# Kernel tuning notes

Hardware: AMD Instinct MI355X
Metric: run time of the kernel (lower is better)

The kernel has to match this reference:

```python
import jax, jax.numpy as jnp
import numpy as np
from jax import lax

K = 3          # kernel_size
OUT = 256      # out_channels
IN_CPG = 256   # in_channels // groups
GROUPS = 1
STRIDE = 1
PAD = 1
DN = ('NCHW', 'OIHW', 'NCHW')


def _bounds(i, n, o):
    return int(np.floor(i * n / o)), int(np.ceil((i + 1) * n / o))


def adaptive_pool2d(x, o, reduce_fn):
    # Faithful torch AdaptiveAvg/MaxPool2d: static bin boundaries.
    H, W = x.shape[2], x.shape[3]
    rows = []
    for i in range(o):
        r0, r1 = _bounds(i, H, o)
        cells = []
        for j in range(o):
            c0, c1 = _bounds(j, W, o)
            cells.append(reduce_fn(x[:, :, r0:r1, c0:c1], axis=(2, 3)))
        rows.append(jnp.stack(cells, axis=-1))
    return jnp.stack(rows, axis=-2)  # (B, C, o, o)


def _gconv(x, w, fg, pad='VALID'):
    return lax.conv_general_dilated(x, w, (1, 1), pad,
                                    dimension_numbers=DN,
                                    feature_group_count=fg)


def setup_inputs() -> dict:
    key = jax.random.key(0)
    ks = jax.random.split(key, 7)
    s = 0.05
    return {
        'x':     jax.random.normal(ks[0], (32, 256, 56, 56), jnp.float32),
        'w1':    jax.random.normal(ks[1], (IN_CPG, GROUPS, 3, 3), jnp.float32) * s,
        'b1':    jax.random.normal(ks[2], (IN_CPG,), jnp.float32) * s,
        'w2':    jax.random.normal(ks[3], (OUT * IN_CPG, 1, 1, 1), jnp.float32) * s,
        'b2':    jax.random.normal(ks[4], (OUT * IN_CPG,), jnp.float32) * s,
        'w_att': jax.random.normal(ks[5], (OUT * IN_CPG, GROUPS, 3, 3), jnp.float32) * s,
        'b_att': jax.random.normal(ks[6], (OUT * IN_CPG,), jnp.float32) * s,
    }


def reference(x, w1, b1, w2, b2, w_att, b_att):
    B, C, H, W = x.shape
    # attention branch: maxpool -> grouped 3x3 conv -> sigmoid
    maxi = adaptive_pool2d(x, K + 2, jnp.max)                    # (B, C, K+2, K+2)
    att = _gconv(maxi, w_att, IN_CPG) + b_att[None, :, None, None]  # (B, OUT*IN_CPG, K, K)
    att = jax.nn.sigmoid(att).reshape(B * OUT, IN_CPG, K, K)
    # weight branch: avgpool -> depthwise 3x3 -> relu -> grouped 1x1
    avg = adaptive_pool2d(x, K + 2, jnp.mean)                    # (B, C, K+2, K+2)
    wgt = jax.nn.relu(_gconv(avg, w1, IN_CPG) + b1[None, :, None, None])  # (B, IN_CPG, K, K)
    wgt = _gconv(wgt, w2, IN_CPG) + b2[None, :, None, None]      # (B, OUT*IN_CPG, K, K)
    wgt = wgt.reshape(B * OUT, IN_CPG, K, K)
    # per-sample dynamic conv as grouped conv with batch-as-groups
    xg = x.reshape(1, B * C, H, W)
    out = lax.conv_general_dilated(xg, wgt * att, (STRIDE, STRIDE),
                                   [(PAD, PAD), (PAD, PAD)],
                                   dimension_numbers=DN,
                                   feature_group_count=GROUPS * B)
    return out.reshape(B, OUT, out.shape[-2], out.shape[-1])
```

## Files before the change

kernel.cpp:

```cpp
#include <hip/hip_runtime.h>
#include <hip/hip_bf16.h>

#define BATCH 32
#define CIN   256
#define OCH   256
#define HW    56
#define PW    58
#define PAREA (PW*PW)
#define PLANE (HW*HW)

typedef float float4v __attribute__((ext_vector_type(4)));
typedef short short8  __attribute__((ext_vector_type(8)));
typedef short short4v __attribute__((ext_vector_type(4)));

__device__ __forceinline__ unsigned short f2bf(float f) {
  union { float f; unsigned u; } v; v.f = f;
  unsigned r = v.u + 0x7fffu + ((v.u >> 16) & 1u);
  return (unsigned short)(r >> 16);
}

__device__ __forceinline__ void gll16(const unsigned short* g, unsigned short* l) {
  __builtin_amdgcn_global_load_lds(
      (const __attribute__((address_space(1))) void*)g,
      (__attribute__((address_space(3))) void*)l,
      16, 0, 0);
}

__global__ __launch_bounds__(512) void poolprep_kernel(
    const float* __restrict__ x, float* __restrict__ avgp,
    float* __restrict__ maxp, unsigned short* __restrict__ xp) {
  __shared__ float pl[4][3140];
  int p = blockIdx.x;
  int L = (p & 7) * 256 + (p >> 3);
  int cg = L & 63, b = L >> 6;
  int tid = threadIdx.x;
  const float* src = x + ((size_t)(b * 256 + cg * 4)) * PLANE;

  float4v v[7];
#pragma unroll
  for (int k = 0; k < 7; ++k) {
    int e = tid + k * 512;
    if (e < 3136) v[k] = *(const float4v*)&src[(size_t)(e / 784) * PLANE + (e % 784) * 4];
  }
#pragma unroll
  for (int k = 0; k < 7; ++k) {
    int e = tid + k * 512;
    if (e < 3136) *(float4v*)&pl[e / 784][(e % 784) * 4] = v[k];
  }
  __syncthreads();

  if (tid < 100) {
    int c = tid / 25, bin = tid % 25;
    int i = bin / 5, j = bin % 5;
    int r0 = (i * HW) / 5, r1 = ((i + 1) * HW + 4) / 5;
    int c0 = (j * HW) / 5, c1 = ((j + 1) * HW + 4) / 5;
    float s = 0.f, m = -1e30f;
    for (int r = r0; r < r1; ++r)
      for (int c2 = c0; c2 < c1; ++c2) {
        float vv = pl[c][r * HW + c2];
        s += vv; m = fmaxf(m, vv);
      }
    size_t o = ((size_t)(b * 256 + cg * 4 + c)) * 25 + bin;
    avgp[o] = s / (float)((r1 - r0) * (c1 - c0));
    maxp[o] = m;
  }

  int ch0 = cg * 4;
  int g32 = ch0 >> 5;
  int cc = (ch0 >> 3) & 3;
  int half = (ch0 >> 2) & 1;
  for (int pi = tid; pi < PLANE; pi += 512) {
    int y = pi / 56, col = pi % 56;
    int pos = (y + 1) * PW + (col + 1);
    short4v w4;
#pragma unroll
    for (int k = 0; k < 4; ++k) w4[k] = (short)f2bf(pl[k][pi]);
    int cph = cc ^ ((pos >> 1) & 3);
    *(short4v*)&xp[((size_t)b * PAREA + pos) * 256 + g32 * 32 + cph * 8 + half * 4] = w4;
  }
}

__global__ __launch_bounds__(256) void wcalc_kernel(
    const float* __restrict__ avgp, const float* __restrict__ maxp,
    const float* __restrict__ w1, const float* __restrict__ b1,
    const float* __restrict__ w2, const float* __restrict__ b2,
    const float* __restrict__ watt, const float* __restrict__ batt,
    unsigned short* __restrict__ Wbf) {
  int blk = blockIdx.x;
  int oc = blk & 255, b = blk >> 8;
  __shared__ float s_avg[25], s_max[25], s_w1[9], s_wgt1[9];
  int tid = threadIdx.x;
  size_t base = ((size_t)b * 256 + oc) * 25;
  if (tid < 25) { s_avg[tid] = avgp[base + tid]; s_max[tid] = maxp[base + tid]; }
  if (tid >= 32 && tid < 41) s_w1[tid - 32] = w1[oc * 9 + (tid - 32)];
  __syncthreads();
  if (tid < 9) {
    int ky = tid / 3, kx = tid % 3;
    float acc = b1[oc];
    for (int u = 0; u < 3; ++u)
      for (int v = 0; v < 3; ++v)
        acc += s_avg[(ky + u) * 5 + kx + v] * s_w1[u * 3 + v];
    s_wgt1[tid] = fmaxf(acc, 0.f);
  }
  __syncthreads();
  int ic = tid;
  size_t g = (size_t)oc * 256 + ic;
  float wa[9];
#pragma unroll
  for (int r = 0; r < 9; ++r) wa[r] = watt[g * 9 + r];
  float ba = batt[g], w2v = w2[g], b2v = b2[g];

  int ocb = oc >> 7, ocl = oc & 127;
  int icb = ic >> 5;
  size_t tilebase = ((size_t)((b * 2 + ocb) * 8 + icb)) * 9;
  size_t elem = (size_t)ocl * 32 + (ic & 31);

#pragma unroll
  for (int r = 0; r < 9; ++r) {
    int ky = r / 3, kx = r % 3;
    float s = ba;
#pragma unroll
    for (int u = 0; u < 3; ++u)
#pragma unroll
      for (int v = 0; v < 3; ++v)
        s += s_max[(ky + u) * 5 + kx + v] * wa[u * 3 + v];
    float att = 1.f / (1.f + __expf(-s));
    float wv = (s_wgt1[r] * w2v + b2v) * att;
    Wbf[(tilebase + r) * 4096 + elem] = f2bf(wv);
  }
}

__global__ __launch_bounds__(256) void border_kernel(unsigned short* __restrict__ xp) {
  int bid = blockIdx.x;
  int b = bid / 228, bi = bid % 228;
  int pos;
  if (bi < 58)       pos = bi;
  else if (bi < 116) pos = 57 * PW + (bi - 58);
  else if (bi < 172) pos = (bi - 116 + 1) * PW;
  else               pos = (bi - 172 + 1) * PW + 57;
  xp[((size_t)b * PAREA + pos) * 256 + threadIdx.x] = 0;
}

__global__ __launch_bounds__(256, 2) void conv_kernel(
    const unsigned short* __restrict__ xp,
    const unsigned short* __restrict__ Wbf,
    float* __restrict__ out) {
  __shared__ unsigned short bpl[2][348 * 32];

  int p = blockIdx.x;
  int L = (p & 7) * 112 + (p >> 3);
  int rt = L % 14; int t2 = L / 14; int ocb = t2 & 1; int b = t2 >> 1;
  int y0 = rt * 4;
  int tid = threadIdx.x;
  int lane = tid & 63, w = tid >> 6;
  int mw = w & 1, nw = w >> 1;
  int quad = lane >> 4, l16 = lane & 15;

  int basepos[7];
#pragma unroll
  for (int nt = 0; nt < 7; ++nt) {
    int n = nw * 112 + nt * 16 + l16;
    basepos[nt] = (n / 56) * PW + (n % 56);
  }

  float4v acc[4][7];
#pragma unroll
  for (int mt = 0; mt < 4; ++mt)
#pragma unroll
    for (int nt = 0; nt < 7; ++nt)
      acc[mt][nt] = (float4v){0.f, 0.f, 0.f, 0.f};

  const size_t xbase = ((size_t)b * PAREA + (size_t)y0 * PW) * 256;
  const unsigned short* wb = Wbf + (size_t)((b * 2 + ocb) * 72) * 4096;
  const int aoff = (mw * 64 + l16) * 32 + quad * 8;

  for (int e = tid; e < 1392; e += 256)
    gll16(&xp[xbase + (size_t)(e >> 2) * 256 + (e & 3) * 8], &bpl[0][e * 8]);
  short8 af0, af1, af2, af3, an0, an1, an2, an3;
  {
    const unsigned short* w0p = wb + aoff;
    af0 = *(const short8*)&w0p[0];    af1 = *(const short8*)&w0p[512];
    af2 = *(const short8*)&w0p[1024]; af3 = *(const short8*)&w0p[1536];
    const unsigned short* w1p = wb + 4096 + aoff;
    an0 = *(const short8*)&w1p[0];    an1 = *(const short8*)&w1p[512];
    an2 = *(const short8*)&w1p[1024]; an3 = *(const short8*)&w1p[1536];
  }
  __syncthreads();

#define RSTEP(R, ICB, CUR, DO2) do {                                            \
    const int _po = ((R) / 3) * PW + ((R) % 3);                                 \
    _Pragma("unroll")                                                           \
    for (int nt = 0; nt < 7; ++nt) {                                            \
      int pr = basepos[nt] + _po;                                               \
      short8 _bf = *(const short8*)&bpl[CUR][pr * 32 + ((quad ^ ((pr >> 1) & 3)) << 3)]; \
      acc[0][nt] = __builtin_amdgcn_mfma_f32_16x16x32_bf16(af0, _bf, acc[0][nt], 0, 0, 0); \
      acc[1][nt] = __builtin_amdgcn_mfma_f32_16x16x32_bf16(af1, _bf, acc[1][nt], 0, 0, 0); \
      acc[2][nt] = __builtin_amdgcn_mfma_f32_16x16x32_bf16(af2, _bf, acc[2][nt], 0, 0, 0); \
      acc[3][nt] = __builtin_amdgcn_mfma_f32_16x16x32_bf16(af3, _bf, acc[3][nt], 0, 0, 0); \
    }                                                                           \
    af0 = an0; af1 = an1; af2 = an2; af3 = an3;                                 \
    if (DO2) {                                                                  \
      const unsigned short* _w = wb + (size_t)((ICB) * 9 + (R) + 2) * 4096 + aoff; \
      an0 = *(const short8*)&_w[0];    an1 = *(const short8*)&_w[512];          \
      an2 = *(const short8*)&_w[1024]; an3 = *(const short8*)&_w[1536];         \
    }                                                                           \
  } while (0)

#pragma unroll 1
  for (int icb = 0; icb < 7; ++icb) {
    int cur = icb & 1;
    for (int e = tid; e < 1392; e += 256)
      gll16(&xp[xbase + (size_t)(e >> 2) * 256 + (icb + 1) * 32 + (e & 3) * 8],
            &bpl[cur ^ 1][e * 8]);
    RSTEP(0, icb, cur, 1); RSTEP(1, icb, cur, 1); RSTEP(2, icb, cur, 1);
    RSTEP(3, icb, cur, 1); RSTEP(4, icb, cur, 1); RSTEP(5, icb, cur, 1);
    RSTEP(6, icb, cur, 1); RSTEP(7, icb, cur, 1); RSTEP(8, icb, cur, 1);
    __syncthreads();
  }
  RSTEP(0, 7, 1, 1); RSTEP(1, 7, 1, 1); RSTEP(2, 7, 1, 1);
  RSTEP(3, 7, 1, 1); RSTEP(4, 7, 1, 1); RSTEP(5, 7, 1, 1);
  RSTEP(6, 7, 1, 1); RSTEP(7, 7, 1, 0); RSTEP(8, 7, 1, 0);
#undef RSTEP

#pragma unroll
  for (int mt = 0; mt < 4; ++mt) {
    int m = ocb * 128 + mw * 64 + mt * 16 + quad * 4;
#pragma unroll
    for (int nt = 0; nt < 7; ++nt) {
      int n = nw * 112 + nt * 16 + l16;
      int yy = y0 + n / 56, xx = n % 56;
      size_t o = (((size_t)b * 256 + m) * 56 + yy) * 56 + xx;
#pragma unroll
      for (int reg = 0; reg < 4; ++reg)
        out[o + (size_t)reg * PLANE] = acc[mt][nt][reg];
    }
  }
}

extern "C" void kernel_launch(void* const* d_in, const int* in_sizes, int n_in,
                              void* d_out, int out_size, void* d_ws, size_t ws_size,
                              hipStream_t stream) {
  const float* x    = (const float*)d_in[0];
  const float* w1   = (const float*)d_in[1];
  const float* b1   = (const float*)d_in[2];
  const float* w2   = (const float*)d_in[3];
  const float* b2   = (const float*)d_in[4];
  const float* watt = (const float*)d_in[5];
  const float* batt = (const float*)d_in[6];
  float* out = (float*)d_out;

  float* avgp = (float*)d_ws;
  float* maxp = avgp + 204800;
  unsigned short* Wbf = (unsigned short*)(maxp + 204800);
  unsigned short* xp  = Wbf + (size_t)32 * 9 * 256 * 256;

  poolprep_kernel<<<BATCH * 64, 512, 0, stream>>>(x, avgp, maxp, xp);
  wcalc_kernel<<<BATCH * OCH, 256, 0, stream>>>(avgp, maxp, w1, b1, w2, b2, watt, batt, Wbf);
  border_kernel<<<BATCH * 228, 256, 0, stream>>>(xp);
  conv_kernel<<<BATCH * 2 * 14, 256, 0, stream>>>(xp, Wbf, out);
}
```

Before: 403.9 us.

## Fuse border zeroing into poolprep and deepen weight/LDS prefetch in conv

The separate border-zeroing kernel is removed, and poolprep now writes the zero halo for its own channel slice, which saves one launch. In the conv kernel the A-operand weight prefetch is deepened from two register sets to three rotating sets, so each load is issued three steps ahead. The global-to-LDS loads for the next channel block are split across the first six filter-tap steps instead of being issued all at once. The aim is to hide global load latency behind MFMA work, at the cost of higher register pressure under 2-wave occupancy bounds.

```diff
diff --git a/kernel.cpp b/kernel.cpp
--- a/kernel.cpp
+++ b/kernel.cpp
@@ -36,12 +36,29 @@
   int tid = threadIdx.x;
   const float* src = x + ((size_t)(b * 256 + cg * 4)) * PLANE;
 
+  int ch0 = cg * 4;
+  int g32 = ch0 >> 5;
+  int cc = (ch0 >> 3) & 3;
+  int half = (ch0 >> 2) & 1;
+
   float4v v[7];
 #pragma unroll
   for (int k = 0; k < 7; ++k) {
     int e = tid + k * 512;
     if (e < 3136) v[k] = *(const float4v*)&src[(size_t)(e / 784) * PLANE + (e % 784) * 4];
   }
+
+  if (tid < 228) {
+    int bi = tid, pos;
+    if (bi < 58)       pos = bi;
+    else if (bi < 116) pos = 57 * PW + (bi - 58);
+    else if (bi < 172) pos = (bi - 116 + 1) * PW;
+    else               pos = (bi - 172 + 1) * PW + 57;
+    int cph = cc ^ ((pos >> 1) & 3);
+    *(short4v*)&xp[((size_t)b * PAREA + pos) * 256 + g32 * 32 + cph * 8 + half * 4] =
+        (short4v){0, 0, 0, 0};
+  }
+
 #pragma unroll
   for (int k = 0; k < 7; ++k) {
     int e = tid + k * 512;
@@ -65,10 +82,6 @@
     maxp[o] = m;
   }
 
-  int ch0 = cg * 4;
-  int g32 = ch0 >> 5;
-  int cc = (ch0 >> 3) & 3;
-  int half = (ch0 >> 2) & 1;
   for (int pi = tid; pi < PLANE; pi += 512) {
     int y = pi / 56, col = pi % 56;
     int pos = (y + 1) * PW + (col + 1);
@@ -130,17 +143,6 @@
   }
 }
 
-__global__ __launch_bounds__(256) void border_kernel(unsigned short* __restrict__ xp) {
-  int bid = blockIdx.x;
-  int b = bid / 228, bi = bid % 228;
-  int pos;
-  if (bi < 58)       pos = bi;
-  else if (bi < 116) pos = 57 * PW + (bi - 58);
-  else if (bi < 172) pos = (bi - 116 + 1) * PW;
-  else               pos = (bi - 172 + 1) * PW + 57;
-  xp[((size_t)b * PAREA + pos) * 256 + threadIdx.x] = 0;
-}
-
 __global__ __launch_bounds__(256, 2) void conv_kernel(
     const unsigned short* __restrict__ xp,
     const unsigned short* __restrict__ Wbf,
@@ -176,50 +178,67 @@
 
   for (int e = tid; e < 1392; e += 256)
     gll16(&xp[xbase + (size_t)(e >> 2) * 256 + (e & 3) * 8], &bpl[0][e * 8]);
-  short8 af0, af1, af2, af3, an0, an1, an2, an3;
+  short8 A0, A1, A2, A3, B0, B1, B2, B3, C0, C1, C2, C3;
   {
     const unsigned short* w0p = wb + aoff;
-    af0 = *(const short8*)&w0p[0];    af1 = *(const short8*)&w0p[512];
-    af2 = *(const short8*)&w0p[1024]; af3 = *(const short8*)&w0p[1536];
+    A0 = *(const short8*)&w0p[0];    A1 = *(const short8*)&w0p[512];
+    A2 = *(const short8*)&w0p[1024]; A3 = *(const short8*)&w0p[1536];
     const unsigned short* w1p = wb + 4096 + aoff;
-    an0 = *(const short8*)&w1p[0];    an1 = *(const short8*)&w1p[512];
-    an2 = *(const short8*)&w1p[1024]; an3 = *(const short8*)&w1p[1536];
-  }
-  __syncthreads();
-
-#define RSTEP(R, ICB, CUR, DO2) do {                                            \
+    B0 = *(const short8*)&w1p[0];    B1 = *(const short8*)&w1p[512];
+    B2 = *(const short8*)&w1p[1024]; B3 = *(const short8*)&w1p[1536];
+    const unsigned short* w2p = wb + 8192 + aoff;
+    C0 = *(const short8*)&w2p[0];    C1 = *(const short8*)&w2p[512];
+    C2 = *(const short8*)&w2p[1024]; C3 = *(const short8*)&w2p[1536];
+  }
+  __syncthreads();
+
+#define RSTEP(R, s0_, s1_, s2_, s3_, ICB, CUR, GLL, REL) do {                   \
+    if (GLL) {                                                                  \
+      int _e = (R) * 256 + tid;                                                 \
+      if (_e < 1392)                                                            \
+        gll16(&xp[xbase + (size_t)(_e >> 2) * 256 + ((ICB) + 1) * 32 + (_e & 3) * 8], \
+              &bpl[(CUR) ^ 1][_e * 8]);                                         \
+    }                                                                           \
     const int _po = ((R) / 3) * PW + ((R) % 3);                                 \
     _Pragma("unroll")                                                           \
     for (int nt = 0; nt < 7; ++nt) {                                            \
       int pr = basepos[nt] + _po;                                               \
       short8 _bf = *(const short8*)&bpl[CUR][pr * 32 + ((quad ^ ((pr >> 1) & 3)) << 3)]; \
-      acc[0][nt] = __builtin_amdgcn_mfma_f32_16x16x32_bf16(af0, _bf, acc[0][nt], 0, 0, 0); \
-      acc[1][nt] = __builtin_amdgcn_mfma_f32_16x16x32_bf16(af1, _bf, acc[1][nt], 0, 0, 0); \
-      acc[2][nt] = __builtin_amdgcn_mfma_f32_16x16x32_bf16(af2, _bf, acc[2][nt], 0, 0, 0); \
-      acc[3][nt] = __builtin_amdgcn_mfma_f32_16x16x32_bf16(af3, _bf, acc[3][nt], 0, 0, 0); \
+      acc[0][nt] = __builtin_amdgcn_mfma_f32_16x16x32_bf16(s0_, _bf, acc[0][nt], 0, 0, 0); \
+      acc[1][nt] = __builtin_amdgcn_mfma_f32_16x16x32_bf16(s1_, _bf, acc[1][nt], 0, 0, 0); \
+      acc[2][nt] = __builtin_amdgcn_mfma_f32_16x16x32_bf16(s2_, _bf, acc[2][nt], 0, 0, 0); \
+      acc[3][nt] = __builtin_amdgcn_mfma_f32_16x16x32_bf16(s3_, _bf, acc[3][nt], 0, 0, 0); \
     }                                                                           \
-    af0 = an0; af1 = an1; af2 = an2; af3 = an3;                                 \
-    if (DO2) {                                                                  \
-      const unsigned short* _w = wb + (size_t)((ICB) * 9 + (R) + 2) * 4096 + aoff; \
-      an0 = *(const short8*)&_w[0];    an1 = *(const short8*)&_w[512];          \
-      an2 = *(const short8*)&_w[1024]; an3 = *(const short8*)&_w[1536];         \
+    if (REL) {                                                                  \
+      const unsigned short* _w = wb + (size_t)((ICB) * 9 + (R) + 3) * 4096 + aoff; \
+      s0_ = *(const short8*)&_w[0];    s1_ = *(const short8*)&_w[512];          \
+      s2_ = *(const short8*)&_w[1024]; s3_ = *(const short8*)&_w[1536];         \
     }                                                                           \
   } while (0)
 
 #pragma unroll 1
   for (int icb = 0; icb < 7; ++icb) {
     int cur = icb & 1;
-    for (int e = tid; e < 1392; e += 256)
-      gll16(&xp[xbase + (size_t)(e >> 2) * 256 + (icb + 1) * 32 + (e & 3) * 8],
-            &bpl[cur ^ 1][e * 8]);
-    RSTEP(0, icb, cur, 1); RSTEP(1, icb, cur, 1); RSTEP(2, icb, cur, 1);
-    RSTEP(3, icb, cur, 1); RSTEP(4, icb, cur, 1); RSTEP(5, icb, cur, 1);
-    RSTEP(6, icb, cur, 1); RSTEP(7, icb, cur, 1); RSTEP(8, icb, cur, 1);
+    RSTEP(0, A0, A1, A2, A3, icb, cur, 1, 1);
+    RSTEP(1, B0, B1, B2, B3, icb, cur, 1, 1);
+    RSTEP(2, C0, C1, C2, C3, icb, cur, 1, 1);
+    RSTEP(3, A0, A1, A2, A3, icb, cur, 1, 1);
+    RSTEP(4, B0, B1, B2, B3, icb, cur, 1, 1);
+    RSTEP(5, C0, C1, C2, C3, icb, cur, 1, 1);
+    RSTEP(6, A0, A1, A2, A3, icb, cur, 0, 1);
+    RSTEP(7, B0, B1, B2, B3, icb, cur, 0, 1);
+    RSTEP(8, C0, C1, C2, C3, icb, cur, 0, 1);
     __syncthreads();
   }
-  RSTEP(0, 7, 1, 1); RSTEP(1, 7, 1, 1); RSTEP(2, 7, 1, 1);
-  RSTEP(3, 7, 1, 1); RSTEP(4, 7, 1, 1); RSTEP(5, 7, 1, 1);
-  RSTEP(6, 7, 1, 1); RSTEP(7, 7, 1, 0); RSTEP(8, 7, 1, 0);
+  RSTEP(0, A0, A1, A2, A3, 7, 1, 0, 1);
+  RSTEP(1, B0, B1, B2, B3, 7, 1, 0, 1);
+  RSTEP(2, C0, C1, C2, C3, 7, 1, 0, 1);
+  RSTEP(3, A0, A1, A2, A3, 7, 1, 0, 1);
+  RSTEP(4, B0, B1, B2, B3, 7, 1, 0, 1);
+  RSTEP(5, C0, C1, C2, C3, 7, 1, 0, 1);
+  RSTEP(6, A0, A1, A2, A3, 7, 1, 0, 0);
+  RSTEP(7, B0, B1, B2, B3, 7, 1, 0, 0);
+  RSTEP(8, C0, C1, C2, C3, 7, 1, 0, 0);
 #undef RSTEP
 
 #pragma unroll
@@ -256,6 +275,5 @@
 
   poolprep_kernel<<<BATCH * 64, 512, 0, stream>>>(x, avgp, maxp, xp);
   wcalc_kernel<<<BATCH * OCH, 256, 0, stream>>>(avgp, maxp, w1, b1, w2, b2, watt, batt, Wbf);
-  border_kernel<<<BATCH * 228, 256, 0, stream>>>(xp);
   conv_kernel<<<BATCH * 2 * 14, 256, 0, stream>>>(xp, Wbf, out);
 }
```

Result: slower. 584.8 us (+44.8%).

## Fold border zeroing into poolprep and retile conv warps to 32x224

Applied to the files above, without the earlier changes.

The border-zeroing kernel is removed; each poolprep block now zeroes its own 4-channel slice of the padded border, saving one launch. The conv kernel changes its warp tiling from 64 oc x 112 pixels to 32 oc x 224 pixels per warp. This halves the A-fragment registers and global weight loads per warp and uses ping-pong weight registers instead of copying them. The cost is twice as many LDS B-fragment reads per MFMA, since each B fragment now feeds only 2 MFMAs instead of 4.

```diff
diff --git a/kernel.cpp b/kernel.cpp
--- a/kernel.cpp
+++ b/kernel.cpp
@@ -36,12 +36,29 @@
   int tid = threadIdx.x;
   const float* src = x + ((size_t)(b * 256 + cg * 4)) * PLANE;
 
+  int ch0 = cg * 4;
+  int g32 = ch0 >> 5;
+  int cc = (ch0 >> 3) & 3;
+  int half = (ch0 >> 2) & 1;
+
   float4v v[7];
 #pragma unroll
   for (int k = 0; k < 7; ++k) {
     int e = tid + k * 512;
     if (e < 3136) v[k] = *(const float4v*)&src[(size_t)(e / 784) * PLANE + (e % 784) * 4];
   }
+
+  if (tid < 228) {
+    int bi = tid, pos;
+    if (bi < 58)       pos = bi;
+    else if (bi < 116) pos = 57 * PW + (bi - 58);
+    else if (bi < 172) pos = (bi - 116 + 1) * PW;
+    else               pos = (bi - 172 + 1) * PW + 57;
+    int cph = cc ^ ((pos >> 1) & 3);
+    *(short4v*)&xp[((size_t)b * PAREA + pos) * 256 + g32 * 32 + cph * 8 + half * 4] =
+        (short4v){0, 0, 0, 0};
+  }
+
 #pragma unroll
   for (int k = 0; k < 7; ++k) {
     int e = tid + k * 512;
@@ -65,10 +82,6 @@
     maxp[o] = m;
   }
 
-  int ch0 = cg * 4;
-  int g32 = ch0 >> 5;
-  int cc = (ch0 >> 3) & 3;
-  int half = (ch0 >> 2) & 1;
   for (int pi = tid; pi < PLANE; pi += 512) {
     int y = pi / 56, col = pi % 56;
     int pos = (y + 1) * PW + (col + 1);
@@ -130,17 +143,6 @@
   }
 }
 
-__global__ __launch_bounds__(256) void border_kernel(unsigned short* __restrict__ xp) {
-  int bid = blockIdx.x;
-  int b = bid / 228, bi = bid % 228;
-  int pos;
-  if (bi < 58)       pos = bi;
-  else if (bi < 116) pos = 57 * PW + (bi - 58);
-  else if (bi < 172) pos = (bi - 116 + 1) * PW;
-  else               pos = (bi - 172 + 1) * PW + 57;
-  xp[((size_t)b * PAREA + pos) * 256 + threadIdx.x] = 0;
-}
-
 __global__ __launch_bounds__(256, 2) void conv_kernel(
     const unsigned short* __restrict__ xp,
     const unsigned short* __restrict__ Wbf,
@@ -153,56 +155,49 @@
   int y0 = rt * 4;
   int tid = threadIdx.x;
   int lane = tid & 63, w = tid >> 6;
-  int mw = w & 1, nw = w >> 1;
   int quad = lane >> 4, l16 = lane & 15;
 
-  int basepos[7];
-#pragma unroll
-  for (int nt = 0; nt < 7; ++nt) {
-    int n = nw * 112 + nt * 16 + l16;
+  int basepos[14];
+#pragma unroll
+  for (int nt = 0; nt < 14; ++nt) {
+    int n = nt * 16 + l16;
     basepos[nt] = (n / 56) * PW + (n % 56);
   }
 
-  float4v acc[4][7];
-#pragma unroll
-  for (int mt = 0; mt < 4; ++mt)
-#pragma unroll
-    for (int nt = 0; nt < 7; ++nt)
+  float4v acc[2][14];
+#pragma unroll
+  for (int mt = 0; mt < 2; ++mt)
+#pragma unroll
+    for (int nt = 0; nt < 14; ++nt)
       acc[mt][nt] = (float4v){0.f, 0.f, 0.f, 0.f};
 
   const size_t xbase = ((size_t)b * PAREA + (size_t)y0 * PW) * 256;
   const unsigned short* wb = Wbf + (size_t)((b * 2 + ocb) * 72) * 4096;
-  const int aoff = (mw * 64 + l16) * 32 + quad * 8;
+  const int aoff = (w * 32 + l16) * 32 + quad * 8;
 
   for (int e = tid; e < 1392; e += 256)
     gll16(&xp[xbase + (size_t)(e >> 2) * 256 + (e & 3) * 8], &bpl[0][e * 8]);
-  short8 af0, af1, af2, af3, an0, an1, an2, an3;
+  short8 s0a, s0b, s1a, s1b;
   {
     const unsigned short* w0p = wb + aoff;
-    af0 = *(const short8*)&w0p[0];    af1 = *(const short8*)&w0p[512];
-    af2 = *(const short8*)&w0p[1024]; af3 = *(const short8*)&w0p[1536];
+    s0a = *(const short8*)&w0p[0];  s0b = *(const short8*)&w0p[512];
     const unsigned short* w1p = wb + 4096 + aoff;
-    an0 = *(const short8*)&w1p[0];    an1 = *(const short8*)&w1p[512];
-    an2 = *(const short8*)&w1p[1024]; an3 = *(const short8*)&w1p[1536];
-  }
-  __syncthreads();
-
-#define RSTEP(R, ICB, CUR, DO2) do {                                            \
+    s1a = *(const short8*)&w1p[0];  s1b = *(const short8*)&w1p[512];
+  }
+  __syncthreads();
+
+#define RSTEP(R, Sa, Sb, ICB, CUR, REL) do {                                    \
     const int _po = ((R) / 3) * PW + ((R) % 3);                                 \
     _Pragma("unroll")                                                           \
-    for (int nt = 0; nt < 7; ++nt) {                                            \
+    for (int nt = 0; nt < 14; ++nt) {                                           \
       int pr = basepos[nt] + _po;                                               \
       short8 _bf = *(const short8*)&bpl[CUR][pr * 32 + ((quad ^ ((pr >> 1) & 3)) << 3)]; \
-      acc[0][nt] = __builtin_amdgcn_mfma_f32_16x16x32_bf16(af0, _bf, acc[0][nt], 0, 0, 0); \
-      acc[1][nt] = __builtin_amdgcn_mfma_f32_16x16x32_bf16(af1, _bf, acc[1][nt], 0, 0, 0); \
-      acc[2][nt] = __builtin_amdgcn_mfma_f32_16x16x32_bf16(af2, _bf, acc[2][nt], 0, 0, 0); \
-      acc[3][nt] = __builtin_amdgcn_mfma_f32_16x16x32_bf16(af3, _bf, acc[3][nt], 0, 0, 0); \
+      acc[0][nt] = __builtin_amdgcn_mfma_f32_16x16x32_bf16(Sa, _bf, acc[0][nt], 0, 0, 0); \
+      acc[1][nt] = __builtin_amdgcn_mfma_f32_16x16x32_bf16(Sb, _bf, acc[1][nt], 0, 0, 0); \
     }                                                                           \
-    af0 = an0; af1 = an1; af2 = an2; af3 = an3;                                 \
-    if (DO2) {                                                                  \
+    if (REL) {                                                                  \
       const unsigned short* _w = wb + (size_t)((ICB) * 9 + (R) + 2) * 4096 + aoff; \
-      an0 = *(const short8*)&_w[0];    an1 = *(const short8*)&_w[512];          \
-      an2 = *(const short8*)&_w[1024]; an3 = *(const short8*)&_w[1536];         \
+      Sa = *(const short8*)&_w[0];  Sb = *(const short8*)&_w[512];              \
     }                                                                           \
   } while (0)
 
@@ -212,22 +207,34 @@
     for (int e = tid; e < 1392; e += 256)
       gll16(&xp[xbase + (size_t)(e >> 2) * 256 + (icb + 1) * 32 + (e & 3) * 8],
             &bpl[cur ^ 1][e * 8]);
-    RSTEP(0, icb, cur, 1); RSTEP(1, icb, cur, 1); RSTEP(2, icb, cur, 1);
-    RSTEP(3, icb, cur, 1); RSTEP(4, icb, cur, 1); RSTEP(5, icb, cur, 1);
-    RSTEP(6, icb, cur, 1); RSTEP(7, icb, cur, 1); RSTEP(8, icb, cur, 1);
+    if (!(icb & 1)) {
+      RSTEP(0, s0a, s0b, icb, cur, 1); RSTEP(1, s1a, s1b, icb, cur, 1);
+      RSTEP(2, s0a, s0b, icb, cur, 1); RSTEP(3, s1a, s1b, icb, cur, 1);
+      RSTEP(4, s0a, s0b, icb, cur, 1); RSTEP(5, s1a, s1b, icb, cur, 1);
+      RSTEP(6, s0a, s0b, icb, cur, 1); RSTEP(7, s1a, s1b, icb, cur, 1);
+      RSTEP(8, s0a, s0b, icb, cur, 1);
+    } else {
+      RSTEP(0, s1a, s1b, icb, cur, 1); RSTEP(1, s0a, s0b, icb, cur, 1);
+      RSTEP(2, s1a, s1b, icb, cur, 1); RSTEP(3, s0a, s0b, icb, cur, 1);
+      RSTEP(4, s1a, s1b, icb, cur, 1); RSTEP(5, s0a, s0b, icb, cur, 1);
+      RSTEP(6, s1a, s1b, icb, cur, 1); RSTEP(7, s0a, s0b, icb, cur, 1);
+      RSTEP(8, s1a, s1b, icb, cur, 1);
+    }
     __syncthreads();
   }
-  RSTEP(0, 7, 1, 1); RSTEP(1, 7, 1, 1); RSTEP(2, 7, 1, 1);
-  RSTEP(3, 7, 1, 1); RSTEP(4, 7, 1, 1); RSTEP(5, 7, 1, 1);
-  RSTEP(6, 7, 1, 1); RSTEP(7, 7, 1, 0); RSTEP(8, 7, 1, 0);
+  RSTEP(0, s1a, s1b, 7, 1, 1); RSTEP(1, s0a, s0b, 7, 1, 1);
+  RSTEP(2, s1a, s1b, 7, 1, 1); RSTEP(3, s0a, s0b, 7, 1, 1);
+  RSTEP(4, s1a, s1b, 7, 1, 1); RSTEP(5, s0a, s0b, 7, 1, 1);
+  RSTEP(6, s1a, s1b, 7, 1, 1); RSTEP(7, s0a, s0b, 7, 1, 0);
+  RSTEP(8, s1a, s1b, 7, 1, 0);
 #undef RSTEP
 
 #pragma unroll
-  for (int mt = 0; mt < 4; ++mt) {
-    int m = ocb * 128 + mw * 64 + mt * 16 + quad * 4;
-#pragma unroll
-    for (int nt = 0; nt < 7; ++nt) {
-      int n = nw * 112 + nt * 16 + l16;
+  for (int mt = 0; mt < 2; ++mt) {
+    int m = ocb * 128 + w * 32 + mt * 16 + quad * 4;
+#pragma unroll
+    for (int nt = 0; nt < 14; ++nt) {
+      int n = nt * 16 + l16;
       int yy = y0 + n / 56, xx = n % 56;
       size_t o = (((size_t)b * 256 + m) * 56 + yy) * 56 + xx;
 #pragma unroll
@@ -256,6 +263,5 @@
 
   poolprep_kernel<<<BATCH * 64, 512, 0, stream>>>(x, avgp, maxp, xp);
   wcalc_kernel<<<BATCH * OCH, 256, 0, stream>>>(avgp, maxp, w1, b1, w2, b2, watt, batt, Wbf);
-  border_kernel<<<BATCH * 228, 256, 0, stream>>>(xp);
   conv_kernel<<<BATCH * 2 * 14, 256, 0, stream>>>(xp, Wbf, out);
 }
```

After: 863.5 us. 2.14x slower.
